# Optimization experiments

Measured on AMD Instinct MI355X. Metric: run time of the kernel, lower is better.

Reference implementation:

```python
import jax, jax.numpy as jnp
import numpy as np

B, S = 128, 512          # batch, padded expression length
D = 256                  # kos/identifier embedding dim (asserted equal)
KIND_D = 8               # token-kind embedding dim
EXPR_D = 512             # expression_encoding_dim
KOS_VOCAB = 256
KIND_VOCAB = 8
NUM_IDS = 8192
PAD_IDX = 0              # padding_idx -> zero embedding row
IDENTIFIER_KIND = 3
KOS_KINDS = (4, 5, 6)    # OPERATOR, SEPARATOR, KEYWORD


def setup_inputs() -> dict:
    key = jax.random.key(0)
    ks = jax.random.split(key, 8)
    token_type = jax.random.randint(ks[0], (B, S), 0, KIND_VOCAB, dtype=jnp.int32)
    kos_token_index = jax.random.randint(ks[1], (B * S,), 0, KOS_VOCAB, dtype=jnp.int32)
    identifier_indices = jax.random.randint(ks[2], (B * S,), 0, NUM_IDS, dtype=jnp.int32)
    encoded_identifiers = jax.random.normal(ks[3], (NUM_IDS, D), jnp.float32)
    kind_emb = jax.random.normal(ks[4], (KIND_VOCAB, KIND_D), jnp.float32).at[PAD_IDX].set(0.0)
    kos_emb = jax.random.normal(ks[5], (KOS_VOCAB, D), jnp.float32).at[PAD_IDX].set(0.0)
    sp = 1.0 / np.sqrt(KIND_D + D)
    W_proj = jax.random.uniform(ks[6], (KIND_D + D, EXPR_D), jnp.float32, -sp, sp)
    b_proj = jnp.zeros((EXPR_D,), jnp.float32)
    sa = 1.0 / np.sqrt(EXPR_D)
    W_add = jax.random.uniform(ks[7], (EXPR_D, EXPR_D), jnp.float32, -sa, sa)
    b_add = jnp.zeros((EXPR_D,), jnp.float32)
    return {
        'token_type': token_type,
        'kos_token_index': kos_token_index,
        'identifier_indices': identifier_indices,
        'encoded_identifiers': encoded_identifiers,
        'kind_emb': kind_emb,
        'kos_emb': kos_emb,
        'W_proj': W_proj,
        'b_proj': b_proj,
        'W_add': W_add,
        'b_add': b_add,
    }


def reference(token_type, kos_token_index, identifier_indices, encoded_identifiers,
              kind_emb, kos_emb, W_proj, b_proj, W_add, b_add):
    # token-kind embedding lookup: [B, S, KIND_D]
    kind_e = kind_emb[token_type]

    flat_kind = token_type.reshape(-1)                       # [B*S]
    is_id = flat_kind == IDENTIFIER_KIND
    is_kos = (flat_kind == KOS_KINDS[0]) | (flat_kind == KOS_KINDS[1]) | (flat_kind == KOS_KINDS[2])

    # embedding-table gathers (sources for masked_scatter, consumed in order)
    id_src = encoded_identifiers[identifier_indices]         # [B*S, D]
    kos_src = kos_emb[kos_token_index]                       # [B*S, D]

    # masked_scatter semantics: the k-th True position gets the k-th source row
    rank_id = jnp.maximum(jnp.cumsum(is_id) - 1, 0)
    rank_kos = jnp.maximum(jnp.cumsum(is_kos) - 1, 0)
    enc = jnp.where(is_id[:, None], id_src[rank_id], jnp.float32(0.0))
    enc = jnp.where(is_kos[:, None], kos_src[rank_kos], enc)
    enc = enc.reshape(B, S, D)

    # concat + 2-layer MLP (dropout is identity in eval mode)
    x = jnp.concatenate([kind_e, enc], axis=-1)              # [B, S, KIND_D + D]
    x = jax.nn.relu(x @ W_proj + b_proj)                     # [B, S, EXPR_D]
    x = jax.nn.relu(x @ W_add + b_add)                       # [B, S, EXPR_D]
    return x
```

## Files before the change

### kernel.cpp

```cpp
#include <hip/hip_runtime.h>
#include <hip/hip_bf16.h>

#define BB 128
#define SS 512
#define NPOS (BB*SS)
#define DD 256
#define KIND_D 8
#define EXPR_D 512
#define KOS_VOCAB 256
#define NUM_IDS 8192
#define IDENTIFIER_KIND 3
#define TROWS 9088

typedef unsigned short u16;
typedef __attribute__((ext_vector_type(8))) short s16x8;
typedef __attribute__((ext_vector_type(8))) unsigned short u16x8;
typedef __attribute__((ext_vector_type(4))) float f32x4;

__device__ __forceinline__ u16 bf16bits(float v) {
    __hip_bfloat16 h = __float2bfloat16(v);
    return *(u16*)&h;
}
__device__ __forceinline__ float bf16tof(u16 b) {
    __hip_bfloat16 h = *(__hip_bfloat16*)&b;
    return __bfloat162float(h);
}

__global__ __launch_bounds__(256) void prep_kernel(const float* __restrict__ W2,
                                                   const float* __restrict__ kind_emb,
                                                   const float* __restrict__ Wp,
                                                   const float* __restrict__ bp,
                                                   const int* __restrict__ token_type,
                                                   u16* __restrict__ Wt,
                                                   u16* __restrict__ Wt1,
                                                   float* __restrict__ kindc,
                                                   int2* __restrict__ blkcnt) {
    __shared__ float tile[32][33];
    __shared__ int swid[4], swkos[4];
    const int bi = blockIdx.x;
    const int t = threadIdx.x;

    if (bi < 256) {
        const int n0 = (bi & 15) * 32;
        const int k0 = (bi >> 4) * 32;
        const int lj = t & 31, li = t >> 5;
        #pragma unroll
        for (int p = 0; p < 4; ++p) {
            int i = li + p * 8;
            tile[i][lj] = W2[(size_t)(k0 + i) * EXPR_D + n0 + lj];
        }
        __syncthreads();
        #pragma unroll
        for (int p = 0; p < 4; ++p) {
            int j = li + p * 8;
            Wt[(size_t)(n0 + j) * EXPR_D + k0 + lj] = bf16bits(tile[lj][j]);
        }
    } else if (bi == 256) {
        #pragma unroll
        for (int rep = 0; rep < 2; ++rep) {
            int j = t + rep * 256;
            float bias = bp[j];
            for (int kind = 0; kind < 8; ++kind) {
                float a = bias;
                #pragma unroll
                for (int d = 0; d < KIND_D; ++d)
                    a = fmaf(kind_emb[kind * KIND_D + d], Wp[d * EXPR_D + j], a);
                kindc[kind * EXPR_D + j] = a;
            }
        }
    } else if (bi < 385) {
        const int idx = bi - 257;
        const int n0 = (idx & 15) * 32;
        const int k0 = (idx >> 4) * 32;
        const float* W1p = Wp + (size_t)KIND_D * EXPR_D;
        const int lj = t & 31, li = t >> 5;
        #pragma unroll
        for (int p = 0; p < 4; ++p) {
            int i = li + p * 8;
            tile[i][lj] = W1p[(size_t)(k0 + i) * EXPR_D + n0 + lj];
        }
        __syncthreads();
        #pragma unroll
        for (int p = 0; p < 4; ++p) {
            int j = li + p * 8;
            Wt1[(size_t)(n0 + j) * DD + k0 + lj] = bf16bits(tile[lj][j]);
        }
    } else {
        const int blk = bi - 385;
        const int lane = t & 63, wave = t >> 6;
        int k = token_type[blk * 256 + t];
        unsigned long long mid  = __ballot(k == IDENTIFIER_KIND);
        unsigned long long mkos = __ballot(k >= 4 && k <= 6);
        if (lane == 0) { swid[wave] = __popcll(mid); swkos[wave] = __popcll(mkos); }
        __syncthreads();
        if (t == 0) {
            int a = 0, c = 0;
            #pragma unroll
            for (int w = 0; w < 4; ++w) { a += swid[w]; c += swkos[w]; }
            blkcnt[blk] = make_int2(a, c);
        }
    }
}

__global__ __launch_bounds__(256) void scatter_kernel(const int* __restrict__ token_type,
                                                      const int2* __restrict__ blkcnt,
                                                      const int* __restrict__ kos_idx,
                                                      const int* __restrict__ id_idx,
                                                      int* __restrict__ sel2) {
    __shared__ int2 sbase;
    __shared__ int swid[4], swkos[4];
    const int b = blockIdx.x, t = threadIdx.x;
    const int lane = t & 63, wave = t >> 6;
    if (t < 64) {
        int a = 0, c = 0;
        for (int i = t; i < b; i += 64) { int2 v = blkcnt[i]; a += v.x; c += v.y; }
        #pragma unroll
        for (int off = 32; off; off >>= 1) { a += __shfl_down(a, off); c += __shfl_down(c, off); }
        if (t == 0) sbase = make_int2(a, c);
    }
    const int idx = b * 256 + t;
    const int k = token_type[idx];
    const bool fid  = (k == IDENTIFIER_KIND);
    const bool fkos = (k >= 4 && k <= 6);
    unsigned long long mid  = __ballot(fid);
    unsigned long long mkos = __ballot(fkos);
    if (lane == 0) { swid[wave] = __popcll(mid); swkos[wave] = __popcll(mkos); }
    __syncthreads();
    int bid = 0, bkos = 0;
    for (int w = 0; w < wave; ++w) { bid += swid[w]; bkos += swkos[w]; }
    unsigned long long below = (1ull << lane) - 1ull;
    int s;
    if (fid)       s = id_idx[sbase.x + bid + __popcll(mid & below)];
    else if (fkos) s = 8192 + (k - 4) * 256 + kos_idx[sbase.y + bkos + __popcll(mkos & below)];
    else           s = 8960 + k;
    sel2[idx] = s;
}

__global__ __launch_bounds__(512, 2) void table_kernel(const float* __restrict__ enc_ids,
                                                       const float* __restrict__ kos_emb,
                                                       const u16* __restrict__ Wt1,
                                                       const float* __restrict__ kindc,
                                                       u16* __restrict__ Thi) {
    __shared__ u16 sAhi[2][128 * 64];
    __shared__ u16 sAlo[2][128 * 64];
    __shared__ u16 sB[2][256 * 64];

    const int t = threadIdx.x;
    const int row0 = blockIdx.x * 128;
    const int col0 = blockIdx.y * 256;

    const int ar = t >> 2;
    const int ac = (t & 3) * 16;
    const int br = t >> 1;
    const int bc = (t & 1) * 32;

    const int arow = row0 + ar;
    const float* Arow;
    bool hasrc = true;
    if (arow < NUM_IDS)        Arow = &enc_ids[(size_t)arow * DD];
    else if (arow < 8960)      Arow = &kos_emb[(size_t)((arow - NUM_IDS) & 255) * DD];
    else { Arow = enc_ids; hasrc = false; }
    const u16* Brow = &Wt1[(size_t)(col0 + br) * DD];

    const int lane = t & 63;
    const int wid  = t >> 6;
    const int wr = wid >> 2, wc = wid & 3;
    const int lrow = lane & 15, lkg = lane >> 4;

    f32x4 acc[4][4];
    #pragma unroll
    for (int mi = 0; mi < 4; ++mi)
        #pragma unroll
        for (int ni = 0; ni < 4; ++ni)
            acc[mi][ni] = (f32x4){0.f, 0.f, 0.f, 0.f};

    f32x4 av[4];
    u16x8 bv[4];

    auto STAGE_ISSUE = [&](int kc) {
        const int kb = kc * 64;
        #pragma unroll
        for (int j = 0; j < 4; ++j)
            av[j] = hasrc ? *(const f32x4*)&Arow[kb + ac + j * 4] : (f32x4){0.f,0.f,0.f,0.f};
        #pragma unroll
        for (int j = 0; j < 4; ++j) bv[j] = *(const u16x8*)&Brow[kb + bc + j * 8];
    };

    auto WRITE = [&](int buf) {
        u16 hi[16], lo[16];
        #pragma unroll
        for (int j = 0; j < 4; ++j)
            #pragma unroll
            for (int e = 0; e < 4; ++e) {
                float r = av[j][e];
                u16 h = bf16bits(r);
                hi[j * 4 + e] = h;
                lo[j * 4 + e] = bf16bits(r - bf16tof(h));
            }
        const int abase = ar * 128;
        const int o0 = abase + ((ac * 2) ^ ((ar & 7) << 4));
        const int o1 = abase + ((ac * 2 + 16) ^ ((ar & 7) << 4));
        *(u16x8*)((char*)sAhi[buf] + o0) = *(const u16x8*)&hi[0];
        *(u16x8*)((char*)sAhi[buf] + o1) = *(const u16x8*)&hi[8];
        *(u16x8*)((char*)sAlo[buf] + o0) = *(const u16x8*)&lo[0];
        *(u16x8*)((char*)sAlo[buf] + o1) = *(const u16x8*)&lo[8];
        const int bbase = br * 128;
        #pragma unroll
        for (int j = 0; j < 4; ++j) {
            int off = bbase + ((bc * 2 + j * 16) ^ ((br & 7) << 4));
            *(u16x8*)((char*)sB[buf] + off) = bv[j];
        }
    };

    auto COMPUTE = [&](int buf) {
        #pragma unroll
        for (int ks = 0; ks < 2; ++ks) {
            s16x8 ah[4], al[4], bbf[4];
            #pragma unroll
            for (int mi = 0; mi < 4; ++mi) {
                int row = wr * 64 + mi * 16 + lrow;
                int off = row * 128 + ((ks * 64 + lkg * 16) ^ ((row & 7) << 4));
                ah[mi] = *(const s16x8*)((const char*)sAhi[buf] + off);
                al[mi] = *(const s16x8*)((const char*)sAlo[buf] + off);
            }
            #pragma unroll
            for (int ni = 0; ni < 4; ++ni) {
                int row = wc * 64 + ni * 16 + lrow;
                int off = row * 128 + ((ks * 64 + lkg * 16) ^ ((row & 7) << 4));
                bbf[ni] = *(const s16x8*)((const char*)sB[buf] + off);
            }
            #pragma unroll
            for (int mi = 0; mi < 4; ++mi)
                #pragma unroll
                for (int ni = 0; ni < 4; ++ni) {
                    acc[mi][ni] = __builtin_amdgcn_mfma_f32_16x16x32_bf16(ah[mi], bbf[ni], acc[mi][ni], 0, 0, 0);
                    acc[mi][ni] = __builtin_amdgcn_mfma_f32_16x16x32_bf16(al[mi], bbf[ni], acc[mi][ni], 0, 0, 0);
                }
        }
    };

    STAGE_ISSUE(0);
    WRITE(0);
    __syncthreads();
    int cur = 0;
    #pragma unroll 1
    for (int kc = 0; kc < 4; ++kc) {
        if (kc < 3) STAGE_ISSUE(kc + 1);
        COMPUTE(cur);
        if (kc < 3) WRITE(cur ^ 1);
        __syncthreads();
        cur ^= 1;
    }

    #pragma unroll
    for (int ni = 0; ni < 4; ++ni) {
        int col = col0 + wc * 64 + ni * 16 + lrow;
        #pragma unroll
        for (int mi = 0; mi < 4; ++mi) {
            int rbase = row0 + wr * 64 + mi * 16 + lkg * 4;
            #pragma unroll
            for (int j = 0; j < 4; ++j) {
                int rg = rbase + j;
                int kind = (rg < NUM_IDS) ? 3
                         : (rg < 8960) ? 4 + ((rg - NUM_IDS) >> 8)
                         : (rg < 8968) ? (rg - 8960) : 0;
                float v = acc[mi][ni][j] + kindc[kind * EXPR_D + col];
                Thi[(size_t)rg * EXPR_D + col] = bf16bits(fmaxf(v, 0.f));
            }
        }
    }
}

__global__ __launch_bounds__(512, 4) void table2_kernel(const u16* __restrict__ Thi,
                                                        const u16* __restrict__ Wt,
                                                        const float* __restrict__ b2,
                                                        float* __restrict__ O) {
    __shared__ u16 sA[2][128 * 32];
    __shared__ u16 sB[2][256 * 32];

    const int t = threadIdx.x;
    const int row0 = blockIdx.x * 128;
    const int col0 = blockIdx.y * 256;

    const int ar = t >> 2;
    const int ac8 = (t & 3) * 8;
    const int br = t >> 1;
    const int bc16 = (t & 1) * 16;

    const u16* Arow = &Thi[(size_t)(row0 + ar) * EXPR_D + ac8];
    const u16* Brow = &Wt[(size_t)(col0 + br) * EXPR_D + bc16];

    const int lane = t & 63;
    const int wid  = t >> 6;
    const int wr = wid >> 2, wc = wid & 3;
    const int lrow = lane & 15, lkg = lane >> 4;

    f32x4 acc[4][4];
    #pragma unroll
    for (int mi = 0; mi < 4; ++mi)
        #pragma unroll
        for (int ni = 0; ni < 4; ++ni)
            acc[mi][ni] = (f32x4){0.f, 0.f, 0.f, 0.f};

    u16x8 av;
    u16x8 bv[2];

    auto STAGE_ISSUE = [&](int kc) {
        const int kb = kc * 32;
        av = *(const u16x8*)&Arow[kb];
        bv[0] = *(const u16x8*)&Brow[kb];
        bv[1] = *(const u16x8*)&Brow[kb + 8];
    };

    auto WRITE = [&](int buf) {
        int aoff = ar * 64 + ((ac8 * 2) ^ ((ar & 3) << 4));
        *(u16x8*)((char*)sA[buf] + aoff) = av;
        #pragma unroll
        for (int j = 0; j < 2; ++j) {
            int boff = br * 64 + ((bc16 * 2 + j * 16) ^ ((br & 3) << 4));
            *(u16x8*)((char*)sB[buf] + boff) = bv[j];
        }
    };

    auto COMPUTE = [&](int buf) {
        s16x8 a[4], b[4];
        #pragma unroll
        for (int mi = 0; mi < 4; ++mi) {
            int row = wr * 64 + mi * 16 + lrow;
            int off = row * 64 + ((lkg * 16) ^ ((row & 3) << 4));
            a[mi] = *(const s16x8*)((const char*)sA[buf] + off);
        }
        #pragma unroll
        for (int ni = 0; ni < 4; ++ni) {
            int row = wc * 64 + ni * 16 + lrow;
            int off = row * 64 + ((lkg * 16) ^ ((row & 3) << 4));
            b[ni] = *(const s16x8*)((const char*)sB[buf] + off);
        }
        #pragma unroll
        for (int mi = 0; mi < 4; ++mi)
            #pragma unroll
            for (int ni = 0; ni < 4; ++ni)
                acc[mi][ni] = __builtin_amdgcn_mfma_f32_16x16x32_bf16(a[mi], b[ni], acc[mi][ni], 0, 0, 0);
    };

    STAGE_ISSUE(0);
    WRITE(0);
    __syncthreads();
    int cur = 0;
    #pragma unroll 1
    for (int kc = 0; kc < 16; ++kc) {
        if (kc < 15) STAGE_ISSUE(kc + 1);
        COMPUTE(cur);
        if (kc < 15) WRITE(cur ^ 1);
        __syncthreads();
        cur ^= 1;
    }

    #pragma unroll
    for (int ni = 0; ni < 4; ++ni) {
        int col = col0 + wc * 64 + ni * 16 + lrow;
        float bias = b2[col];
        #pragma unroll
        for (int mi = 0; mi < 4; ++mi) {
            int rbase = row0 + wr * 64 + mi * 16 + lkg * 4;
            #pragma unroll
            for (int j = 0; j < 4; ++j)
                O[(size_t)(rbase + j) * EXPR_D + col] = fmaxf(acc[mi][ni][j] + bias, 0.f);
        }
    }
}

__global__ __launch_bounds__(256) void gather_kernel(const int* __restrict__ sel2,
                                                     const float* __restrict__ O,
                                                     float* __restrict__ out) {
    const int t = threadIdx.x;
    const int lane = t & 63, wave = t >> 6;
    const int base = blockIdx.x * 16;
    int rows[4];
    #pragma unroll
    for (int i = 0; i < 4; ++i) rows[i] = sel2[base + i * 4 + wave];
    f32x4 v0[4], v1[4];
    #pragma unroll
    for (int i = 0; i < 4; ++i) {
        const f32x4* src = (const f32x4*)&O[(size_t)rows[i] * EXPR_D];
        v0[i] = src[lane];
        v1[i] = src[lane + 64];
    }
    #pragma unroll
    for (int i = 0; i < 4; ++i) {
        const int pos = base + i * 4 + wave;
        f32x4* dst = (f32x4*)&out[(size_t)pos * EXPR_D];
        __builtin_nontemporal_store(v0[i], &dst[lane]);
        __builtin_nontemporal_store(v1[i], &dst[lane + 64]);
    }
}

extern "C" void kernel_launch(void* const* d_in, const int* in_sizes, int n_in,
                              void* d_out, int out_size, void* d_ws, size_t ws_size,
                              hipStream_t stream) {
    const int*   token_type = (const int*)d_in[0];
    const int*   kos_idx    = (const int*)d_in[1];
    const int*   id_idx     = (const int*)d_in[2];
    const float* enc_ids    = (const float*)d_in[3];
    const float* kind_emb   = (const float*)d_in[4];
    const float* kos_emb    = (const float*)d_in[5];
    const float* Wp         = (const float*)d_in[6];
    const float* bp         = (const float*)d_in[7];
    const float* W2         = (const float*)d_in[8];
    const float* b2         = (const float*)d_in[9];
    float* out = (float*)d_out;

    char* ws = (char*)d_ws;
    int*   sel2   = (int*)ws;
    float* kindc  = (float*)(ws + 262144);
    int2*  blkcnt = (int2*)(ws + 278528);
    u16*   Wt     = (u16*)(ws + 282624);
    u16*   Wt1    = (u16*)(ws + 806912);
    u16*   Thi    = (u16*)(ws + 1069056);
    float* O      = (float*)(ws + 10375168);

    hipLaunchKernelGGL(prep_kernel, dim3(641), dim3(256), 0, stream,
                       W2, kind_emb, Wp, bp, token_type, Wt, Wt1, kindc, blkcnt);
    hipLaunchKernelGGL(scatter_kernel, dim3(256), dim3(256), 0, stream,
                       token_type, blkcnt, kos_idx, id_idx, sel2);
    hipLaunchKernelGGL(table_kernel, dim3(TROWS / 128, EXPR_D / 256), dim3(512), 0, stream,
                       enc_ids, kos_emb, Wt1, kindc, Thi);
    hipLaunchKernelGGL(table2_kernel, dim3(TROWS / 128, EXPR_D / 256), dim3(512), 0, stream,
                       Thi, Wt, b2, O);
    hipLaunchKernelGGL(gather_kernel, dim3(NPOS / 16), dim3(256), 0, stream,
                       sel2, O, out);
}
```

Before: 75.83 us.

## Fuse scatter into table kernel, halve table2 tile rows, store table as bf16

The scatter work is folded into the first table GEMM launch as extra blocks, which removes one kernel launch. The second GEMM now uses 64-row tiles, doubling its block count for better occupancy across CUs. It writes its output table in bf16 instead of fp32, so the gather kernel reads half as many bytes and converts back to fp32. The bf16 rounding of final outputs adds precision loss beyond the earlier bf16 intermediates.

Result: slower. 104.1 us (+37.3%).

```diff
diff --git a/kernel.cpp b/kernel.cpp
--- a/kernel.cpp
+++ b/kernel.cpp
@@ -102,52 +102,61 @@
     }
 }
 
-__global__ __launch_bounds__(256) void scatter_kernel(const int* __restrict__ token_type,
-                                                      const int2* __restrict__ blkcnt,
-                                                      const int* __restrict__ kos_idx,
-                                                      const int* __restrict__ id_idx,
-                                                      int* __restrict__ sel2) {
-    __shared__ int2 sbase;
-    __shared__ int swid[4], swkos[4];
-    const int b = blockIdx.x, t = threadIdx.x;
-    const int lane = t & 63, wave = t >> 6;
-    if (t < 64) {
-        int a = 0, c = 0;
-        for (int i = t; i < b; i += 64) { int2 v = blkcnt[i]; a += v.x; c += v.y; }
-        #pragma unroll
-        for (int off = 32; off; off >>= 1) { a += __shfl_down(a, off); c += __shfl_down(c, off); }
-        if (t == 0) sbase = make_int2(a, c);
-    }
-    const int idx = b * 256 + t;
-    const int k = token_type[idx];
-    const bool fid  = (k == IDENTIFIER_KIND);
-    const bool fkos = (k >= 4 && k <= 6);
-    unsigned long long mid  = __ballot(fid);
-    unsigned long long mkos = __ballot(fkos);
-    if (lane == 0) { swid[wave] = __popcll(mid); swkos[wave] = __popcll(mkos); }
-    __syncthreads();
-    int bid = 0, bkos = 0;
-    for (int w = 0; w < wave; ++w) { bid += swid[w]; bkos += swkos[w]; }
-    unsigned long long below = (1ull << lane) - 1ull;
-    int s;
-    if (fid)       s = id_idx[sbase.x + bid + __popcll(mid & below)];
-    else if (fkos) s = 8192 + (k - 4) * 256 + kos_idx[sbase.y + bkos + __popcll(mkos & below)];
-    else           s = 8960 + k;
-    sel2[idx] = s;
-}
-
 __global__ __launch_bounds__(512, 2) void table_kernel(const float* __restrict__ enc_ids,
                                                        const float* __restrict__ kos_emb,
                                                        const u16* __restrict__ Wt1,
                                                        const float* __restrict__ kindc,
-                                                       u16* __restrict__ Thi) {
+                                                       const int* __restrict__ token_type,
+                                                       const int2* __restrict__ blkcnt,
+                                                       const int* __restrict__ kos_idx,
+                                                       const int* __restrict__ id_idx,
+                                                       u16* __restrict__ Thi,
+                                                       int* __restrict__ sel2) {
     __shared__ u16 sAhi[2][128 * 64];
     __shared__ u16 sAlo[2][128 * 64];
     __shared__ u16 sB[2][256 * 64];
-
+    __shared__ int sw8id[8], sw8kos[8];
+    __shared__ int sb[4];
+
+    const int bi = blockIdx.x;
     const int t = threadIdx.x;
-    const int row0 = blockIdx.x * 128;
-    const int col0 = blockIdx.y * 256;
+
+    if (bi >= 142) {
+        const int q = bi - 142;
+        const int lane = t & 63, wave8 = t >> 6;
+        const int h = t >> 8;
+        if (t < 64) {
+            int a = 0, c = 0;
+            for (int i = t; i < 2 * q; i += 64) { int2 v = blkcnt[i]; a += v.x; c += v.y; }
+            #pragma unroll
+            for (int off = 32; off; off >>= 1) { a += __shfl_down(a, off); c += __shfl_down(c, off); }
+            if (t == 0) {
+                int2 e = blkcnt[2 * q];
+                sb[0] = a; sb[1] = c;
+                sb[2] = a + e.x; sb[3] = c + e.y;
+            }
+        }
+        const int idx = q * 512 + t;
+        const int k = token_type[idx];
+        const bool fid  = (k == IDENTIFIER_KIND);
+        const bool fkos = (k >= 4 && k <= 6);
+        unsigned long long mid  = __ballot(fid);
+        unsigned long long mkos = __ballot(fkos);
+        if (lane == 0) { sw8id[wave8] = __popcll(mid); sw8kos[wave8] = __popcll(mkos); }
+        __syncthreads();
+        int bid = 0, bkos = 0;
+        for (int w = 4 * h; w < wave8; ++w) { bid += sw8id[w]; bkos += sw8kos[w]; }
+        unsigned long long below = (1ull << lane) - 1ull;
+        int s;
+        if (fid)       s = id_idx[sb[2 * h] + bid + __popcll(mid & below)];
+        else if (fkos) s = 8192 + (k - 4) * 256 + kos_idx[sb[2 * h + 1] + bkos + __popcll(mkos & below)];
+        else           s = 8960 + k;
+        sel2[idx] = s;
+        return;
+    }
+
+    const int row0 = (bi % 71) * 128;
+    const int col0 = (bi / 71) * 256;
 
     const int ar = t >> 2;
     const int ac = (t & 3) * 16;
@@ -274,15 +283,16 @@
 __global__ __launch_bounds__(512, 4) void table2_kernel(const u16* __restrict__ Thi,
                                                         const u16* __restrict__ Wt,
                                                         const float* __restrict__ b2,
-                                                        float* __restrict__ O) {
-    __shared__ u16 sA[2][128 * 32];
+                                                        u16* __restrict__ Obf) {
+    __shared__ u16 sA[2][64 * 32];
     __shared__ u16 sB[2][256 * 32];
 
     const int t = threadIdx.x;
-    const int row0 = blockIdx.x * 128;
+    const int row0 = blockIdx.x * 64;
     const int col0 = blockIdx.y * 256;
 
-    const int ar = t >> 2;
+    const bool doA = (t < 256);
+    const int ar = (t & 255) >> 2;
     const int ac8 = (t & 3) * 8;
     const int br = t >> 1;
     const int bc16 = (t & 1) * 16;
@@ -295,9 +305,9 @@
     const int wr = wid >> 2, wc = wid & 3;
     const int lrow = lane & 15, lkg = lane >> 4;
 
-    f32x4 acc[4][4];
-    #pragma unroll
-    for (int mi = 0; mi < 4; ++mi)
+    f32x4 acc[2][4];
+    #pragma unroll
+    for (int mi = 0; mi < 2; ++mi)
         #pragma unroll
         for (int ni = 0; ni < 4; ++ni)
             acc[mi][ni] = (f32x4){0.f, 0.f, 0.f, 0.f};
@@ -307,14 +317,16 @@
 
     auto STAGE_ISSUE = [&](int kc) {
         const int kb = kc * 32;
-        av = *(const u16x8*)&Arow[kb];
+        if (doA) av = *(const u16x8*)&Arow[kb];
         bv[0] = *(const u16x8*)&Brow[kb];
         bv[1] = *(const u16x8*)&Brow[kb + 8];
     };
 
     auto WRITE = [&](int buf) {
-        int aoff = ar * 64 + ((ac8 * 2) ^ ((ar & 3) << 4));
-        *(u16x8*)((char*)sA[buf] + aoff) = av;
+        if (doA) {
+            int aoff = ar * 64 + ((ac8 * 2) ^ ((ar & 3) << 4));
+            *(u16x8*)((char*)sA[buf] + aoff) = av;
+        }
         #pragma unroll
         for (int j = 0; j < 2; ++j) {
             int boff = br * 64 + ((bc16 * 2 + j * 16) ^ ((br & 3) << 4));
@@ -323,10 +335,10 @@
     };
 
     auto COMPUTE = [&](int buf) {
-        s16x8 a[4], b[4];
-        #pragma unroll
-        for (int mi = 0; mi < 4; ++mi) {
-            int row = wr * 64 + mi * 16 + lrow;
+        s16x8 a[2], b[4];
+        #pragma unroll
+        for (int mi = 0; mi < 2; ++mi) {
+            int row = wr * 32 + mi * 16 + lrow;
             int off = row * 64 + ((lkg * 16) ^ ((row & 3) << 4));
             a[mi] = *(const s16x8*)((const char*)sA[buf] + off);
         }
@@ -337,7 +349,7 @@
             b[ni] = *(const s16x8*)((const char*)sB[buf] + off);
         }
         #pragma unroll
-        for (int mi = 0; mi < 4; ++mi)
+        for (int mi = 0; mi < 2; ++mi)
             #pragma unroll
             for (int ni = 0; ni < 4; ++ni)
                 acc[mi][ni] = __builtin_amdgcn_mfma_f32_16x16x32_bf16(a[mi], b[ni], acc[mi][ni], 0, 0, 0);
@@ -361,17 +373,17 @@
         int col = col0 + wc * 64 + ni * 16 + lrow;
         float bias = b2[col];
         #pragma unroll
-        for (int mi = 0; mi < 4; ++mi) {
-            int rbase = row0 + wr * 64 + mi * 16 + lkg * 4;
+        for (int mi = 0; mi < 2; ++mi) {
+            int rbase = row0 + wr * 32 + mi * 16 + lkg * 4;
             #pragma unroll
             for (int j = 0; j < 4; ++j)
-                O[(size_t)(rbase + j) * EXPR_D + col] = fmaxf(acc[mi][ni][j] + bias, 0.f);
+                Obf[(size_t)(rbase + j) * EXPR_D + col] = bf16bits(fmaxf(acc[mi][ni][j] + bias, 0.f));
         }
     }
 }
 
 __global__ __launch_bounds__(256) void gather_kernel(const int* __restrict__ sel2,
-                                                     const float* __restrict__ O,
+                                                     const u16* __restrict__ Obf,
                                                      float* __restrict__ out) {
     const int t = threadIdx.x;
     const int lane = t & 63, wave = t >> 6;
@@ -379,19 +391,22 @@
     int rows[4];
     #pragma unroll
     for (int i = 0; i < 4; ++i) rows[i] = sel2[base + i * 4 + wave];
-    f32x4 v0[4], v1[4];
-    #pragma unroll
-    for (int i = 0; i < 4; ++i) {
-        const f32x4* src = (const f32x4*)&O[(size_t)rows[i] * EXPR_D];
-        v0[i] = src[lane];
-        v1[i] = src[lane + 64];
-    }
+    u16x8 r[4];
+    #pragma unroll
+    for (int i = 0; i < 4; ++i)
+        r[i] = *(const u16x8*)&Obf[(size_t)rows[i] * EXPR_D + lane * 8];
     #pragma unroll
     for (int i = 0; i < 4; ++i) {
         const int pos = base + i * 4 + wave;
-        f32x4* dst = (f32x4*)&out[(size_t)pos * EXPR_D];
-        __builtin_nontemporal_store(v0[i], &dst[lane]);
-        __builtin_nontemporal_store(v1[i], &dst[lane + 64]);
+        float* dst = &out[(size_t)pos * EXPR_D + lane * 8];
+        f32x4 lo, hi;
+        #pragma unroll
+        for (int e = 0; e < 4; ++e) {
+            lo[e] = bf16tof((u16)r[i][e]);
+            hi[e] = bf16tof((u16)r[i][e + 4]);
+        }
+        __builtin_nontemporal_store(lo, (f32x4*)dst);
+        __builtin_nontemporal_store(hi, (f32x4*)(dst + 4));
     }
 }
 
@@ -417,16 +432,15 @@
     u16*   Wt     = (u16*)(ws + 282624);
     u16*   Wt1    = (u16*)(ws + 806912);
     u16*   Thi    = (u16*)(ws + 1069056);
-    float* O      = (float*)(ws + 10375168);
+    u16*   Obf    = (u16*)(ws + 10375168);
 
     hipLaunchKernelGGL(prep_kernel, dim3(641), dim3(256), 0, stream,
                        W2, kind_emb, Wp, bp, token_type, Wt, Wt1, kindc, blkcnt);
-    hipLaunchKernelGGL(scatter_kernel, dim3(256), dim3(256), 0, stream,
-                       token_type, blkcnt, kos_idx, id_idx, sel2);
-    hipLaunchKernelGGL(table_kernel, dim3(TROWS / 128, EXPR_D / 256), dim3(512), 0, stream,
-                       enc_ids, kos_emb, Wt1, kindc, Thi);
-    hipLaunchKernelGGL(table2_kernel, dim3(TROWS / 128, EXPR_D / 256), dim3(512), 0, stream,
-                       Thi, Wt, b2, O);
+    hipLaunchKernelGGL(table_kernel, dim3(142 + 128), dim3(512), 0, stream,
+                       enc_ids, kos_emb, Wt1, kindc, token_type, blkcnt, kos_idx, id_idx,
+                       Thi, sel2);
+    hipLaunchKernelGGL(table2_kernel, dim3(TROWS / 64, EXPR_D / 256), dim3(512), 0, stream,
+                       Thi, Wt, b2, Obf);
     hipLaunchKernelGGL(gather_kernel, dim3(NPOS / 16), dim3(256), 0, stream,
-                       sel2, O, out);
-}
+                       sel2, Obf, out);
+}
```
